# Kernel tuning notes

Hardware: AMD Instinct MI355X
Metric: run time of the kernel (lower is better)

## Reference

```python
import jax, jax.numpy as jnp
import numpy as np
from jax.scipy.special import i0

# --- NUFFT adjoint (Kaiser-Bessel gridding) configuration ---
N = 512            # image side (image_shape)
K = 2 * N
M = 200_000        # n_measurements (visibilities)
B = 8              # batch of measurement vectors
J = 6              # gridding kernel width (plan uses (6, 6))
BETA = 2.34 * J


def setup_inputs() -> dict:
    key = jax.random.key(0)
    k1, k2, k3 = jax.random.split(key, 3)
    # uv coordinates in [-pi, pi) radians per pixel (standard NUFFT convention)
    uv = jax.random.uniform(k1, (M, 2), jnp.float32, -np.pi, np.pi)
    y_real = jax.random.normal(k2, (B, M), jnp.float32)
    y_imag = jax.random.normal(k3, (B, M), jnp.float32)
    weights = jnp.ones((M,), jnp.float32)  # measurement_weights
    return {"y_real": y_real, "y_imag": y_imag, "uv": uv, "weights": weights}


def _grid_1d(coord):
    """Per-axis gridding indices and Kaiser-Bessel weights.

    coord: (M,) frequencies in [-pi, pi). Returns idx (M, J) int32 grid
    columns (wrapped mod K) and w (M, J) float32 kernel weights.
    """
    k = coord / (2.0 * np.pi) * K            # grid units, in [-K/2, K/2)
    km = jnp.floor(k - J / 2.0)              # leftmost neighbor base
    j = jnp.arange(1, J + 1, dtype=k.dtype)
    pts = km[:, None] + j                    # (M, J) grid points covered
    d = k[:, None] - pts                     # signed distance, |d| <= J/2
    arg = jnp.maximum(1.0 - (2.0 * d / J) ** 2, 0.0)
    w = i0(BETA * jnp.sqrt(arg)) / i0(jnp.float32(BETA))
    idx = jnp.mod(pts, K).astype(jnp.int32)
    return idx, w.astype(jnp.float32)


def _deapod(n):
    """Gridding-correction (inverse FT of the KB kernel) at image pixels."""
    x = (jnp.arange(n, dtype=jnp.float32) - n / 2.0) / K
    t = BETA ** 2 - (np.pi * J * x) ** 2
    st = jnp.sqrt(jnp.abs(t))
    num = jnp.where(t > 0, jnp.sinh(st), jnp.sin(st))
    return num / jnp.maximum(st, 1e-6)


def reference(y_real, y_imag, uv, weights):
    y = (y_real + 1j * y_imag).astype(jnp.complex64) * weights  # (B, M)

    ix, wx = _grid_1d(uv[:, 0])  # (M, J)
    iy, wy = _grid_1d(uv[:, 1])  # (M, J)

    # Separable 6x6 kernel: outer products per measurement
    flat_idx = (ix[:, :, None] * K + iy[:, None, :]).reshape(-1)        # (M*J*J,)
    w2 = (wx[:, :, None] * wy[:, None, :]).reshape(M, J * J)            # (M, 36)
    vals = (y[:, :, None] * w2[None]).reshape(B, -1)                    # (B, M*36)

    # Scatter-add onto the oversampled grid (duplicate indices accumulate)
    grid = jnp.zeros((B, K * K), jnp.complex64).at[:, flat_idx].add(vals)
    grid = grid.reshape(B, K, K)

    # Unnormalized inverse FFT (adjoint of the forward FFT), shift to center
    img = jnp.fft.fftshift(jnp.fft.ifft2(grid), axes=(-2, -1)) * (K * K)

    # Crop central N x N region and de-apodize
    s = (K - N) // 2
    img_c = jnp.real(img[:, s:s + N, s:s + N])
    apod = _deapod(N)
    return img_c / (apod[:, None] * apod[None, :])
```

## Files before the change

### kernel.cpp

```cpp
#include <hip/hip_runtime.h>
#include <math.h>

#define KGRID 1024
#define NIMG  512
#define JW    6
#define BETAF 14.04f
#define NB    8
#define TS    8
#define NBIN  16384
#define CAP   96

__device__ __forceinline__ float i0f_dev(float x) {
    float ax = fabsf(x);
    if (ax < 3.75f) {
        float z = ax * (1.0f / 3.75f);
        z = z * z;
        return 1.0f + z * (3.5156229f + z * (3.0899424f + z * (1.2067492f +
               z * (0.2659732f + z * (0.0360768f + z * 0.0045813f)))));
    } else {
        float z = 3.75f / ax;
        float p = 0.39894228f + z * (0.01328592f + z * (0.00225319f + z * (-0.00157565f +
                  z * (0.00916281f + z * (-0.02057706f + z * (0.02635537f +
                  z * (-0.01647633f + z * 0.00392377f)))))));
        return expf(ax) * rsqrtf(ax) * p;
    }
}

__global__ __launch_bounds__(256) void prep_kernel(
    const float* __restrict__ yr, const float* __restrict__ yi,
    const float* __restrict__ uv, const float* __restrict__ wts,
    float4* __restrict__ yF4, float4* __restrict__ pnt,
    int* __restrict__ cnt, int* __restrict__ list, int M)
{
    int m = blockIdx.x * 256 + threadIdx.x;
    if (m >= M) return;

    if (m == 0) {
        float4 z = make_float4(0.f, 0.f, 0.f, 0.f);
        #pragma unroll
        for (int q = 0; q < 4; q++) { pnt[(size_t)M * 4 + q] = z; yF4[(size_t)M * 4 + q] = z; }
    }

    float inv = 1.0f / i0f_dev(BETAF);
    float s2 = inv * inv;

    #pragma unroll
    for (int bp = 0; bp < 4; bp++) {
        int b0 = 2 * bp;
        yF4[(size_t)m * 4 + bp] = make_float4(
            yr[(size_t)b0 * M + m],       yi[(size_t)b0 * M + m],
            yr[(size_t)(b0 + 1) * M + m], yi[(size_t)(b0 + 1) * M + m]);
    }

    float u = uv[2 * m], v = uv[2 * m + 1];
    float sc = wts[m] * s2;
    const float c2g = (float)KGRID / 6.283185307179586f;
    float kx = u * c2g, ky = v * c2g;
    float kmx = floorf(kx - 3.0f), kmy = floorf(ky - 3.0f);
    int x0m = (((int)kmx + 1) + 1024) & 1023;
    int y0m = (((int)kmy + 1) + 1024) & 1023;

    float wx[JW], wy[JW];
    #pragma unroll
    for (int j = 0; j < JW; j++) {
        float dx = kx - kmx - 1.0f - (float)j;
        float rx = dx * (1.0f / 3.0f);
        float ax = fmaxf(1.0f - rx * rx, 0.0f);
        wx[j] = i0f_dev(BETAF * sqrtf(ax)) * sc;
        float dy = ky - kmy - 1.0f - (float)j;
        float ry = dy * (1.0f / 3.0f);
        float ay = fmaxf(1.0f - ry * ry, 0.0f);
        wy[j] = i0f_dev(BETAF * sqrtf(ay));
    }

    float4* p = pnt + (size_t)m * 4;
    p[0] = make_float4(wx[0], wx[1], wx[2], wx[3]);
    p[1] = make_float4(wx[4], wx[5], __int_as_float(x0m), __int_as_float(y0m));
    p[2] = make_float4(wy[0], wy[1], wy[2], wy[3]);
    p[3] = make_float4(wy[4], wy[5], 0.0f, 0.0f);

    int txA = x0m >> 3, txB = (txA + 1) & 127;
    int tyA = y0m >> 3, tyB = (tyA + 1) & 127;
    bool bx = (x0m & 7) >= 3;
    bool by = (y0m & 7) >= 3;

    #define PUSH(tx, ty) { int bin = ((tx) << 7) | (ty);                 \
                           int slot = atomicAdd(&cnt[bin], 1);           \
                           if (slot < CAP) list[bin * CAP + slot] = m; }
    PUSH(txA, tyA);
    if (by)  PUSH(txA, tyB);
    if (bx) { PUSH(txB, tyA); if (by) PUSH(txB, tyB); }
    #undef PUSH
}

__global__ __launch_bounds__(256) void grid_tile(
    const float* __restrict__ pnt1, const float4* __restrict__ yF4,
    const int* __restrict__ cnt, const int* __restrict__ list,
    float2* __restrict__ gP, int M)
{
    int lane = threadIdx.x & 63;
    int wid  = threadIdx.x >> 6;
    int tile = blockIdx.x * 4 + wid;
    int tx0 = (tile >> 7) << 3;
    int ty0 = (tile & 127) << 3;
    int lx = lane >> 3, ly = lane & 7;
    int slot = lane & 15;

    float2 acc[NB];
    #pragma unroll
    for (int b = 0; b < NB; b++) acc[b] = make_float2(0.f, 0.f);

    int n = cnt[tile]; if (n > CAP) n = CAP;
    const int* lst = list + tile * CAP;

    int lv0 = (lane < n) ? lst[lane] : M;
    int lv1 = (64 + lane < n && 64 + lane < CAP) ? lst[64 + lane] : M;

    #define FETCH_M(i) __builtin_amdgcn_readlane(((i) < 64) ? lv0 : lv1, (i) & 63)

    int   mA = FETCH_M(0), mB = FETCH_M(1);
    float pwA = pnt1[(size_t)mA * 16 + slot];
    float pwB = pnt1[(size_t)mB * 16 + slot];
    float4 yA0 = yF4[(size_t)mA * 4 + 0], yA1 = yF4[(size_t)mA * 4 + 1],
           yA2 = yF4[(size_t)mA * 4 + 2], yA3 = yF4[(size_t)mA * 4 + 3];
    float4 yB0 = yF4[(size_t)mB * 4 + 0], yB1 = yF4[(size_t)mB * 4 + 1],
           yB2 = yF4[(size_t)mB * 4 + 2], yB3 = yF4[(size_t)mB * 4 + 3];

    for (int i = 0; i < n; i++) {
        int mC = FETCH_M(i + 2);
        float pwC = pnt1[(size_t)mC * 16 + slot];
        float4 yC0 = yF4[(size_t)mC * 4 + 0], yC1 = yF4[(size_t)mC * 4 + 1],
               yC2 = yF4[(size_t)mC * 4 + 2], yC3 = yF4[(size_t)mC * 4 + 3];

        int pwb = __float_as_int(pwA);
        int x0 = __builtin_amdgcn_readlane(pwb, 6);
        int y0 = __builtin_amdgcn_readlane(pwb, 7);
        int j1 = (tx0 + lx - x0) & 1023;
        int j2 = (ty0 + ly - y0) & 1023;
        int i1 = (j1 < 6) ? j1 : 15;
        int i2 = (j2 < 6) ? (j2 + 8) : 14;
        float wx = __int_as_float(__builtin_amdgcn_ds_bpermute(i1 << 2, pwb));
        float wy = __int_as_float(__builtin_amdgcn_ds_bpermute(i2 << 2, pwb));
        float w = wx * wy;

        acc[0].x = fmaf(w, yA0.x, acc[0].x); acc[0].y = fmaf(w, yA0.y, acc[0].y);
        acc[1].x = fmaf(w, yA0.z, acc[1].x); acc[1].y = fmaf(w, yA0.w, acc[1].y);
        acc[2].x = fmaf(w, yA1.x, acc[2].x); acc[2].y = fmaf(w, yA1.y, acc[2].y);
        acc[3].x = fmaf(w, yA1.z, acc[3].x); acc[3].y = fmaf(w, yA1.w, acc[3].y);
        acc[4].x = fmaf(w, yA2.x, acc[4].x); acc[4].y = fmaf(w, yA2.y, acc[4].y);
        acc[5].x = fmaf(w, yA2.z, acc[5].x); acc[5].y = fmaf(w, yA2.w, acc[5].y);
        acc[6].x = fmaf(w, yA3.x, acc[6].x); acc[6].y = fmaf(w, yA3.y, acc[6].y);
        acc[7].x = fmaf(w, yA3.z, acc[7].x); acc[7].y = fmaf(w, yA3.w, acc[7].y);

        pwA = pwB; yA0 = yB0; yA1 = yB1; yA2 = yB2; yA3 = yB3;
        pwB = pwC; yB0 = yC0; yB1 = yC1; yB2 = yC2; yB3 = yC3;
    }
    #undef FETCH_M

    size_t cell = ((size_t)(tx0 + lx) << 10) + (size_t)(ty0 + ly);
    #pragma unroll
    for (int b = 0; b < NB; b++)
        gP[((size_t)b << 20) + cell] = acc[b];
}

__device__ __forceinline__ void fft1024_inv(float2* X, float2* Y, const float2* W, int tid)
{
    float2* src = X;
    float2* dst = Y;
    #pragma unroll
    for (int stage = 0; stage < 10; stage++) {
        const int s = 1 << stage;
        __syncthreads();
        #pragma unroll
        for (int h = 0; h < 2; h++) {
            int t  = tid + (h << 8);
            int sp = t & ~(s - 1);
            float2 c0 = src[t];
            float2 c1 = src[t + 512];
            float2 sum = make_float2(c0.x + c1.x, c0.y + c1.y);
            float2 dif = make_float2(c0.x - c1.x, c0.y - c1.y);
            float2 w = W[sp];
            dst[t + sp]     = sum;
            dst[t + sp + s] = make_float2(w.x * dif.x - w.y * dif.y,
                                          w.x * dif.y + w.y * dif.x);
        }
        float2* tmp = src; src = dst; dst = tmp;
    }
    __syncthreads();
}

__global__ __launch_bounds__(256) void fft_pass1(const float2* __restrict__ gP,
                                                 float2* __restrict__ T)
{
    __shared__ float2 A[1024];
    __shared__ float2 Bb[1024];
    __shared__ float2 W[512];
    __shared__ float2 R[4][512];

    int blk = blockIdx.x;
    int p   = blk >> 8;
    int k1g = blk & 255;
    int tid = threadIdx.x;

    #pragma unroll
    for (int h = 0; h < 2; h++) {
        int j = tid + (h << 8);
        float sn, cn;
        __sincosf(6.283185307179586f * (float)j * (1.0f / 1024.0f), &sn, &cn);
        W[j] = make_float2(cn, sn);
    }

    const float2* gA = gP + ((size_t)(2 * p)     << 20);
    const float2* gB = gP + ((size_t)(2 * p + 1) << 20);

    for (int r = 0; r < 4; r++) {
        int k1  = (k1g << 2) + r;
        int nk1 = (1024 - k1) & 1023;
        const float2* rA  = gA + ((size_t)k1  << 10);
        const float2* rAn = gA + ((size_t)nk1 << 10);
        const float2* rB  = gB + ((size_t)k1  << 10);
        const float2* rBn = gB + ((size_t)nk1 << 10);
        __syncthreads();
        #pragma unroll
        for (int h = 0; h < 4; h++) {
            int k2  = tid + (h << 8);
            int nk2 = (1024 - k2) & 1023;
            float2 va  = rA[k2];
            float2 van = rAn[nk2];
            float2 vb  = rB[k2];
            float2 vbn = rBn[nk2];
            A[k2] = make_float2(0.5f * (va.x + van.x) - 0.5f * (vb.y - vbn.y),
                                0.5f * (va.y - van.y) + 0.5f * (vb.x + vbn.x));
        }
        fft1024_inv(A, Bb, W, tid);
        #pragma unroll
        for (int h = 0; h < 2; h++) {
            int xo2 = tid + (h << 8);
            R[r][xo2] = A[(xo2 + 768) & 1023];
        }
    }
    __syncthreads();

    #pragma unroll
    for (int h = 0; h < 2; h++) {
        int xo2 = tid + (h << 8);
        float2 f0 = R[0][xo2], f1 = R[1][xo2], f2 = R[2][xo2], f3 = R[3][xo2];
        float4* d4 = (float4*)(T + (((size_t)p * 512 + xo2) << 10) + (k1g << 2));
        d4[0] = make_float4(f0.x, f0.y, f1.x, f1.y);
        d4[1] = make_float4(f2.x, f2.y, f3.x, f3.y);
    }
}

__device__ __forceinline__ float apodf(int n) {
    float x  = ((float)n - 256.0f) * (1.0f / 1024.0f);
    float px = 3.14159265358979f * 6.0f * x;
    float t  = BETAF * BETAF - px * px;
    float st = sqrtf(fabsf(t));
    float num = (t > 0.0f) ? sinhf(st) : __sinf(st);
    return num / fmaxf(st, 1e-6f);
}

__global__ __launch_bounds__(256) void fft_pass2(const float2* __restrict__ T,
                                                 float* __restrict__ out)
{
    __shared__ float2 A[1024];
    __shared__ float2 Bb[1024];
    __shared__ float2 W[512];
    __shared__ float2 R[4][512];

    int blk = blockIdx.x;
    int p   = blk >> 7;
    int xg  = blk & 127;
    int tid = threadIdx.x;

    #pragma unroll
    for (int h = 0; h < 2; h++) {
        int j = tid + (h << 8);
        float sn, cn;
        __sincosf(6.283185307179586f * (float)j * (1.0f / 1024.0f), &sn, &cn);
        W[j] = make_float2(cn, sn);
    }

    float a2[4];
    #pragma unroll
    for (int r = 0; r < 4; r++) a2[r] = apodf((xg << 2) + r);

    for (int r = 0; r < 4; r++) {
        int xo2 = (xg << 2) + r;
        const float2* row = T + (((size_t)p * 512 + xo2) << 10);
        __syncthreads();
        #pragma unroll
        for (int h = 0; h < 4; h++) { int i = tid + (h << 8); A[i] = row[i]; }
        fft1024_inv(A, Bb, W, tid);
        #pragma unroll
        for (int h = 0; h < 2; h++) {
            int xo1 = tid + (h << 8);
            float2 v = A[(xo1 + 768) & 1023];
            R[r][xo1] = make_float2(v.x / a2[r], v.y / a2[r]);
        }
    }
    __syncthreads();

    int b0 = 2 * p;
    #pragma unroll
    for (int h = 0; h < 2; h++) {
        int xo1 = tid + (h << 8);
        float inva1 = 1.0f / apodf(xo1);
        float2 f0 = R[0][xo1], f1 = R[1][xo1], f2 = R[2][xo1], f3 = R[3][xo1];
        float4* o0 = (float4*)(out + (((size_t)b0 * 512 + xo1) << 9) + (xg << 2));
        float4* o1 = (float4*)(out + (((size_t)(b0 + 1) * 512 + xo1) << 9) + (xg << 2));
        *o0 = make_float4(f0.x * inva1, f1.x * inva1, f2.x * inva1, f3.x * inva1);
        *o1 = make_float4(f0.y * inva1, f1.y * inva1, f2.y * inva1, f3.y * inva1);
    }
}

extern "C" void kernel_launch(void* const* d_in, const int* in_sizes, int n_in,
                              void* d_out, int out_size, void* d_ws, size_t ws_size,
                              hipStream_t stream)
{
    const float* yr  = (const float*)d_in[0];
    const float* yi  = (const float*)d_in[1];
    const float* uv  = (const float*)d_in[2];
    const float* wts = (const float*)d_in[3];

    int M = in_sizes[3];

    float2* gP = (float2*)d_ws;
    char*   p2 = (char*)d_ws + ((size_t)64 << 20);
    float2* T  = (float2*)p2;
    int*    cnt  = (int*)p2;
    int*    list = (int*)(p2 + 65536);
    float4* yF4  = (float4*)(p2 + 6553600);
    float4* pnt  = (float4*)(p2 + 19500032);

    hipMemsetAsync(cnt, 0, NBIN * sizeof(int), stream);
    prep_kernel<<<dim3((M + 255) / 256), dim3(256), 0, stream>>>(
        yr, yi, uv, wts, yF4, pnt, cnt, list, M);
    grid_tile<<<dim3(NBIN / 4), dim3(256), 0, stream>>>(
        (const float*)pnt, (const float4*)yF4, cnt, list, gP, M);
    fft_pass1<<<dim3(4 * 256), dim3(256), 0, stream>>>(gP, T);
    fft_pass2<<<dim3(4 * 128), dim3(256), 0, stream>>>(T, (float*)d_out);
}
```

Before: 189.3 us.

## Store gridded data and FFT intermediate in fp16, deepen prefetch, pair rows

The oversampled grid and the intermediate between the two FFT passes are now stored as half2 instead of float2, halving global memory traffic for the grid write and both FFT passes. The gridding loop prefetches three measurements ahead instead of two. The first FFT pass now handles rows k and their mirror partners in the same block, with half as many blocks and 8 rows each. Half precision storage adds rounding error and overflow risk on the grid sums, which may break the accuracy tolerance.

```diff
diff --git a/kernel.cpp b/kernel.cpp
--- a/kernel.cpp
+++ b/kernel.cpp
@@ -1,4 +1,5 @@
 #include <hip/hip_runtime.h>
+#include <hip/hip_fp16.h>
 #include <math.h>
 
 #define KGRID 1024
@@ -6,7 +7,6 @@
 #define JW    6
 #define BETAF 14.04f
 #define NB    8
-#define TS    8
 #define NBIN  16384
 #define CAP   96
 
@@ -96,7 +96,7 @@
 __global__ __launch_bounds__(256) void grid_tile(
     const float* __restrict__ pnt1, const float4* __restrict__ yF4,
     const int* __restrict__ cnt, const int* __restrict__ list,
-    float2* __restrict__ gP, int M)
+    __half2* __restrict__ gH, int M)
 {
     int lane = threadIdx.x & 63;
     int wid  = threadIdx.x >> 6;
@@ -118,19 +118,22 @@
 
     #define FETCH_M(i) __builtin_amdgcn_readlane(((i) < 64) ? lv0 : lv1, (i) & 63)
 
-    int   mA = FETCH_M(0), mB = FETCH_M(1);
+    int   mA = FETCH_M(0), mB = FETCH_M(1), mC = FETCH_M(2);
     float pwA = pnt1[(size_t)mA * 16 + slot];
     float pwB = pnt1[(size_t)mB * 16 + slot];
+    float pwC = pnt1[(size_t)mC * 16 + slot];
     float4 yA0 = yF4[(size_t)mA * 4 + 0], yA1 = yF4[(size_t)mA * 4 + 1],
            yA2 = yF4[(size_t)mA * 4 + 2], yA3 = yF4[(size_t)mA * 4 + 3];
     float4 yB0 = yF4[(size_t)mB * 4 + 0], yB1 = yF4[(size_t)mB * 4 + 1],
            yB2 = yF4[(size_t)mB * 4 + 2], yB3 = yF4[(size_t)mB * 4 + 3];
+    float4 yC0 = yF4[(size_t)mC * 4 + 0], yC1 = yF4[(size_t)mC * 4 + 1],
+           yC2 = yF4[(size_t)mC * 4 + 2], yC3 = yF4[(size_t)mC * 4 + 3];
 
     for (int i = 0; i < n; i++) {
-        int mC = FETCH_M(i + 2);
-        float pwC = pnt1[(size_t)mC * 16 + slot];
-        float4 yC0 = yF4[(size_t)mC * 4 + 0], yC1 = yF4[(size_t)mC * 4 + 1],
-               yC2 = yF4[(size_t)mC * 4 + 2], yC3 = yF4[(size_t)mC * 4 + 3];
+        int mD = FETCH_M(i + 3);
+        float pwD = pnt1[(size_t)mD * 16 + slot];
+        float4 yD0 = yF4[(size_t)mD * 4 + 0], yD1 = yF4[(size_t)mD * 4 + 1],
+               yD2 = yF4[(size_t)mD * 4 + 2], yD3 = yF4[(size_t)mD * 4 + 3];
 
         int pwb = __float_as_int(pwA);
         int x0 = __builtin_amdgcn_readlane(pwb, 6);
@@ -154,13 +157,14 @@
 
         pwA = pwB; yA0 = yB0; yA1 = yB1; yA2 = yB2; yA3 = yB3;
         pwB = pwC; yB0 = yC0; yB1 = yC1; yB2 = yC2; yB3 = yC3;
+        pwC = pwD; yC0 = yD0; yC1 = yD1; yC2 = yD2; yC3 = yD3;
     }
     #undef FETCH_M
 
     size_t cell = ((size_t)(tx0 + lx) << 10) + (size_t)(ty0 + ly);
     #pragma unroll
     for (int b = 0; b < NB; b++)
-        gP[((size_t)b << 20) + cell] = acc[b];
+        gH[((size_t)b << 20) + cell] = __float22half2_rn(acc[b]);
 }
 
 __device__ __forceinline__ void fft1024_inv(float2* X, float2* Y, const float2* W, int tid)
@@ -189,17 +193,17 @@
     __syncthreads();
 }
 
-__global__ __launch_bounds__(256) void fft_pass1(const float2* __restrict__ gP,
-                                                 float2* __restrict__ T)
+__global__ __launch_bounds__(256) void fft_pass1(const __half2* __restrict__ gH,
+                                                 __half2* __restrict__ T)
 {
     __shared__ float2 A[1024];
     __shared__ float2 Bb[1024];
     __shared__ float2 W[512];
-    __shared__ float2 R[4][512];
+    __shared__ __half2 R[8][512];
 
     int blk = blockIdx.x;
-    int p   = blk >> 8;
-    int k1g = blk & 255;
+    int p   = blk >> 7;
+    int g   = blk & 127;
     int tid = threadIdx.x;
 
     #pragma unroll
@@ -210,25 +214,25 @@
         W[j] = make_float2(cn, sn);
     }
 
-    const float2* gA = gP + ((size_t)(2 * p)     << 20);
-    const float2* gB = gP + ((size_t)(2 * p + 1) << 20);
-
-    for (int r = 0; r < 4; r++) {
-        int k1  = (k1g << 2) + r;
+    const __half2* gA = gH + ((size_t)(2 * p)     << 20);
+    const __half2* gB = gH + ((size_t)(2 * p + 1) << 20);
+
+    for (int f = 0; f < 8; f++) {
+        int k1  = (f < 4) ? (4 * g + f) : (1020 - 4 * g + (f - 4));
         int nk1 = (1024 - k1) & 1023;
-        const float2* rA  = gA + ((size_t)k1  << 10);
-        const float2* rAn = gA + ((size_t)nk1 << 10);
-        const float2* rB  = gB + ((size_t)k1  << 10);
-        const float2* rBn = gB + ((size_t)nk1 << 10);
+        const __half2* rA  = gA + ((size_t)k1  << 10);
+        const __half2* rAn = gA + ((size_t)nk1 << 10);
+        const __half2* rB  = gB + ((size_t)k1  << 10);
+        const __half2* rBn = gB + ((size_t)nk1 << 10);
         __syncthreads();
         #pragma unroll
         for (int h = 0; h < 4; h++) {
             int k2  = tid + (h << 8);
             int nk2 = (1024 - k2) & 1023;
-            float2 va  = rA[k2];
-            float2 van = rAn[nk2];
-            float2 vb  = rB[k2];
-            float2 vbn = rBn[nk2];
+            float2 va  = __half22float2(rA[k2]);
+            float2 van = __half22float2(rAn[nk2]);
+            float2 vb  = __half22float2(rB[k2]);
+            float2 vbn = __half22float2(rBn[nk2]);
             A[k2] = make_float2(0.5f * (va.x + van.x) - 0.5f * (vb.y - vbn.y),
                                 0.5f * (va.y - van.y) + 0.5f * (vb.x + vbn.x));
         }
@@ -236,7 +240,7 @@
         #pragma unroll
         for (int h = 0; h < 2; h++) {
             int xo2 = tid + (h << 8);
-            R[r][xo2] = A[(xo2 + 768) & 1023];
+            R[f][xo2] = __float22half2_rn(A[(xo2 + 768) & 1023]);
         }
     }
     __syncthreads();
@@ -244,10 +248,14 @@
     #pragma unroll
     for (int h = 0; h < 2; h++) {
         int xo2 = tid + (h << 8);
-        float2 f0 = R[0][xo2], f1 = R[1][xo2], f2 = R[2][xo2], f3 = R[3][xo2];
-        float4* d4 = (float4*)(T + (((size_t)p * 512 + xo2) << 10) + (k1g << 2));
-        d4[0] = make_float4(f0.x, f0.y, f1.x, f1.y);
-        d4[1] = make_float4(f2.x, f2.y, f3.x, f3.y);
+        __half2* Trow = T + (((size_t)p * 512 + xo2) << 10);
+        int4 q0, q1;
+        q0.x = *(const int*)&R[0][xo2]; q0.y = *(const int*)&R[1][xo2];
+        q0.z = *(const int*)&R[2][xo2]; q0.w = *(const int*)&R[3][xo2];
+        q1.x = *(const int*)&R[4][xo2]; q1.y = *(const int*)&R[5][xo2];
+        q1.z = *(const int*)&R[6][xo2]; q1.w = *(const int*)&R[7][xo2];
+        *(int4*)(Trow + 4 * g)          = q0;
+        *(int4*)(Trow + (1020 - 4 * g)) = q1;
     }
 }
 
@@ -260,7 +268,7 @@
     return num / fmaxf(st, 1e-6f);
 }
 
-__global__ __launch_bounds__(256) void fft_pass2(const float2* __restrict__ T,
+__global__ __launch_bounds__(256) void fft_pass2(const __half2* __restrict__ T,
                                                  float* __restrict__ out)
 {
     __shared__ float2 A[1024];
@@ -287,10 +295,13 @@
 
     for (int r = 0; r < 4; r++) {
         int xo2 = (xg << 2) + r;
-        const float2* row = T + (((size_t)p * 512 + xo2) << 10);
+        const __half2* row = T + (((size_t)p * 512 + xo2) << 10);
         __syncthreads();
         #pragma unroll
-        for (int h = 0; h < 4; h++) { int i = tid + (h << 8); A[i] = row[i]; }
+        for (int h = 0; h < 4; h++) {
+            int i = tid + (h << 8);
+            A[i] = __half22float2(row[i]);
+        }
         fft1024_inv(A, Bb, W, tid);
         #pragma unroll
         for (int h = 0; h < 2; h++) {
@@ -325,9 +336,9 @@
 
     int M = in_sizes[3];
 
-    float2* gP = (float2*)d_ws;
-    char*   p2 = (char*)d_ws + ((size_t)64 << 20);
-    float2* T  = (float2*)p2;
+    __half2* gH = (__half2*)d_ws;
+    __half2* T  = (__half2*)((char*)d_ws + ((size_t)32 << 20));
+    char*    p2 = (char*)d_ws + ((size_t)64 << 20);
     int*    cnt  = (int*)p2;
     int*    list = (int*)(p2 + 65536);
     float4* yF4  = (float4*)(p2 + 6553600);
@@ -337,7 +348,7 @@
     prep_kernel<<<dim3((M + 255) / 256), dim3(256), 0, stream>>>(
         yr, yi, uv, wts, yF4, pnt, cnt, list, M);
     grid_tile<<<dim3(NBIN / 4), dim3(256), 0, stream>>>(
-        (const float*)pnt, (const float4*)yF4, cnt, list, gP, M);
-    fft_pass1<<<dim3(4 * 256), dim3(256), 0, stream>>>(gP, T);
+        (const float*)pnt, (const float4*)yF4, cnt, list, gH, M);
+    fft_pass1<<<dim3(4 * 128), dim3(256), 0, stream>>>(gH, T);
     fft_pass2<<<dim3(4 * 128), dim3(256), 0, stream>>>(T, (float*)d_out);
 }
```

Measured after the change: 192.4 us. Within noise of the previous version (+1.7%).
